# Performance work log

Measured on AMD Instinct MI355X. Metric: run time of the kernel, lower is better.

## Reference

```python
import jax, jax.numpy as jnp
import numpy as np

B, L = 4, 1024
D_MODEL, D_STATE, D_CONV, EXPAND, NUM_HEADS = 512, 64, 4, 2, 8
HEADDIM = 64
D_INNER = EXPAND * D_MODEL          # 1024
NH = D_INNER // HEADDIM             # 16 SSM heads
D_IN_PROJ = 2 * D_INNER + 2 * D_STATE + NH
CONV_DIM = D_INNER + 2 * D_STATE
D_FF = D_MODEL * EXPAND
ADH = D_MODEL // NUM_HEADS          # attn head dim


def setup_inputs() -> dict:
    ks = iter(jax.random.split(jax.random.key(0), 40))
    def rn(shape, s=0.02):
        return jax.random.normal(next(ks), shape, jnp.float32) * s
    return dict(
        x=jax.random.normal(next(ks), (B, L, D_MODEL), jnp.float32),
        g1=jnp.ones(D_MODEL), b1=jnp.zeros(D_MODEL),
        W_in=rn((D_MODEL, D_IN_PROJ)), b_in=jnp.zeros(D_IN_PROJ),
        conv_w=rn((CONV_DIM, D_CONV), 0.1), conv_b=jnp.zeros(CONV_DIM),
        dt_bias=rn((NH,), 0.1), A_log=jnp.zeros(NH), D_skip=jnp.ones(NH),
        gnorm=jnp.ones(D_INNER),
        W_out=rn((D_INNER, D_MODEL)), b_out=jnp.zeros(D_MODEL),
        ga=jnp.ones(D_MODEL), ba=jnp.zeros(D_MODEL),
        Wqkv=rn((D_MODEL, 3 * D_MODEL)), bqkv=jnp.zeros(3 * D_MODEL),
        Wo=rn((D_MODEL, D_MODEL)), bo=jnp.zeros(D_MODEL),
        g2=jnp.ones(D_MODEL), b2=jnp.zeros(D_MODEL),
        W1=rn((D_MODEL, 2 * D_FF)), b1f=jnp.zeros(2 * D_FF),
        W2=rn((D_FF, D_MODEL)), b2f=jnp.zeros(D_MODEL),
    )


def _ln(x, g, b, eps=1e-5):
    mu = x.mean(-1, keepdims=True)
    v = ((x - mu) ** 2).mean(-1, keepdims=True)
    return (x - mu) * jax.lax.rsqrt(v + eps) * g + b


def _ssm(h, W_in, b_in, conv_w, conv_b, dt_bias, A_log, D_skip, gnorm, W_out, b_out):
    # Mamba2: in_proj -> [z | xBC | dt]
    zxbcdt = h @ W_in + b_in
    z = zxbcdt[..., :D_INNER]
    xBC = zxbcdt[..., D_INNER:D_INNER + CONV_DIM]
    dt = jax.nn.softplus(zxbcdt[..., -NH:] + dt_bias)          # [B,L,H]
    # causal depthwise conv (width D_CONV) + SiLU
    xp = jnp.pad(xBC, ((0, 0), (D_CONV - 1, 0), (0, 0)))
    conv = conv_b + sum(xp[:, k:k + L, :] * conv_w[:, k] for k in range(D_CONV))
    xBC = jax.nn.silu(conv)
    bsz = h.shape[0]
    xs = xBC[..., :D_INNER].reshape(bsz, L, NH, HEADDIM)       # [B,L,H,P]
    Bm = xBC[..., D_INNER:D_INNER + D_STATE]                   # [B,L,N]
    Cm = xBC[..., D_INNER + D_STATE:]                          # [B,L,N]
    dA = jnp.exp(dt * (-jnp.exp(A_log)))                       # [B,L,H]
    dtx = dt[..., None] * xs                                   # [B,L,H,P]

    def step(hs, t):
        dA_t, dtx_t, B_t, C_t = t
        hs = hs * dA_t[..., None, None] + dtx_t[..., None] * B_t[:, None, None, :]
        return hs, jnp.einsum('bhpn,bn->bhp', hs, C_t)

    h0 = jnp.zeros((bsz, NH, HEADDIM, D_STATE), h.dtype)
    _, ys = jax.lax.scan(step, h0, (dA.swapaxes(0, 1), dtx.swapaxes(0, 1),
                                     Bm.swapaxes(0, 1), Cm.swapaxes(0, 1)))
    y = ys.swapaxes(0, 1) + D_skip[None, None, :, None] * xs   # [B,L,H,P]
    y = y.reshape(bsz, L, D_INNER) * jax.nn.silu(z)            # gated
    y = y * jax.lax.rsqrt(jnp.mean(y * y, -1, keepdims=True) + 1e-5) * gnorm  # RMSNormGated
    return y @ W_out + b_out


def _attn(h, Wqkv, bqkv, Wo, bo):
    qkv = h @ Wqkv + bqkv
    q, k, v = jnp.split(qkv, 3, axis=-1)
    bsz = h.shape[0]
    rs = lambda t: t.reshape(bsz, L, NUM_HEADS, ADH)
    q, k, v = rs(q), rs(k), rs(v)
    scale = jnp.float32(1.0 / np.sqrt(ADH))
    att = jax.nn.softmax(jnp.einsum('blhd,bmhd->bhlm', q, k) * scale, axis=-1)
    o = jnp.einsum('bhlm,bmhd->blhd', att, v).reshape(bsz, L, D_MODEL)
    return o @ Wo + bo


def _fwd(x, g1, b1, W_in, b_in, conv_w, conv_b, dt_bias, A_log, D_skip, gnorm,
         W_out, b_out, ga, ba, Wqkv, bqkv, Wo, bo, g2, b2, W1, b1f, W2, b2f):
    x = x + _ssm(_ln(x, g1, b1), W_in, b_in, conv_w, conv_b, dt_bias, A_log,
                 D_skip, gnorm, W_out, b_out)
    x = x + _attn(_ln(x, ga, ba), Wqkv, bqkv, Wo, bo)
    h3 = _ln(x, g2, b2)
    x1, x2 = jnp.split(h3 @ W1 + b1f, 2, axis=-1)
    return x + (jax.nn.gelu(x1, approximate=False) * x2) @ W2 + b2f


def reference(x, g1, b1, W_in, b_in, conv_w, conv_b, dt_bias, A_log, D_skip, gnorm,
              W_out, b_out, ga, ba, Wqkv, bqkv, Wo, bo, g2, b2, W1, b1f, W2, b2f):
    return _fwd(x, g1, b1, W_in, b_in, conv_w, conv_b, dt_bias, A_log, D_skip, gnorm,
                W_out, b_out, ga, ba, Wqkv, bqkv, Wo, bo, g2, b2, W1, b1f, W2, b2f)
```

## Files before the change

kernel.cpp:

```cpp
#include <hip/hip_runtime.h>
#include <hip/hip_bf16.h>
#include <math.h>


#define L_      1024
#define DM      512
#define DSTATE  64
#define DCONV   4
#define DINNER  1024
#define NH_     16
#define DINPROJ 2192
#define CONVDIM 1152
#define ROWS    4096
#define LC      64
#define NC      16

typedef float  f32x4  __attribute__((ext_vector_type(4)));
typedef __bf16 bf16x8 __attribute__((ext_vector_type(8)));
typedef short  short8 __attribute__((ext_vector_type(8)));
using bf16 = __hip_bfloat16;

static __device__ __forceinline__ float b2f(ushort u) { return __uint_as_float((unsigned)u << 16); }
static __device__ __forceinline__ ushort f2b(float f) {
  return __builtin_bit_cast(unsigned short, __float2bfloat16(f));
}
static __device__ __forceinline__ void gload16(const void* g, void* l) {
  __builtin_amdgcn_global_load_lds((const __attribute__((address_space(1))) void*)g,
                                   (__attribute__((address_space(3))) void*)l, 16, 0, 0);
}
static __device__ __forceinline__ int swz(int row, int col) {
  return row * 64 + ((((col >> 3) ^ (row & 7)) << 3) | (col & 7));
}

struct TcAll {
  const float* W[6];
  ushort* WT[6];
  int K[6], N[6], Nalloc[6], nbx[6], perm[6];
  int start[7];
};
__global__ __launch_bounds__(256) void tcall_k(TcAll d) {
  int bid = blockIdx.x;
  int i = 0;
  #pragma unroll
  for (int t = 1; t < 6; ++t) if (bid >= d.start[t]) i = t;
  int local = bid - d.start[i];
  int bx = (local % d.nbx[i]) * 32, by = (local / d.nbx[i]) * 32;
  const float* W = d.W[i];
  ushort* WT = d.WT[i];
  int K = d.K[i], N = d.N[i], Nalloc = d.Nalloc[i], pm = d.perm[i];
  __shared__ ushort tile[32][33];
  int tx = threadIdx.x & 31, ty = threadIdx.x >> 5;
  #pragma unroll
  for (int r = ty; r < 32; r += 8) {
    int gk = by + r, gn = bx + tx;
    tile[r][tx] = (gk < K && gn < N) ? f2b(W[(size_t)gk * N + gn]) : (ushort)0;
  }
  __syncthreads();
  #pragma unroll
  for (int r = ty; r < 32; r += 8) {
    int gn = bx + r, gk = by + tx;
    if (gn < Nalloc && gk < K) {
      int gn2 = gn;
      if (pm) gn2 = (gn < 1024) ? ((gn >> 4) * 32 + (gn & 15))
                                : (((gn - 1024) >> 4) * 32 + 16 + ((gn - 1024) & 15));
      WT[(size_t)gn2 * K + gk] = tile[tx][r];
    }
  }
}

__global__ __launch_bounds__(256) void ln512(const float* __restrict__ in, const float* __restrict__ g,
                                             const float* __restrict__ be, bf16* __restrict__ out) {
  int row = blockIdx.x, tid = threadIdx.x;
  const float* x = in + (size_t)row * DM;
  float v0 = x[tid], v1 = x[tid + 256];
  float s = v0 + v1, sq = v0 * v0 + v1 * v1;
  __shared__ float red[4][2];
  __shared__ float bc[2];
  int lane = tid & 63, w = tid >> 6;
  #pragma unroll
  for (int o = 32; o; o >>= 1) { s += __shfl_down(s, o); sq += __shfl_down(sq, o); }
  if (lane == 0) { red[w][0] = s; red[w][1] = sq; }
  __syncthreads();
  if (tid == 0) {
    bc[0] = red[0][0] + red[1][0] + red[2][0] + red[3][0];
    bc[1] = red[0][1] + red[1][1] + red[2][1] + red[3][1];
  }
  __syncthreads();
  float mu = bc[0] * (1.f / DM);
  float var = bc[1] * (1.f / DM) - mu * mu;
  float rs = rsqrtf(var + 1e-5f);
  out[(size_t)row * DM + tid] = __float2bfloat16((v0 - mu) * rs * g[tid] + be[tid]);
  out[(size_t)row * DM + tid + 256] =
      __float2bfloat16((v1 - mu) * rs * g[tid + 256] + be[tid + 256]);
}

template <int OMODE, int BM>
__global__ __launch_bounds__(256) void gemmT(const ushort* __restrict__ A, long lda, long sA1,
                                             const ushort* __restrict__ Bw, long ldb, long sB1,
                                             const float* __restrict__ bias,
                                             void* __restrict__ Cp, long ldc, long sC1,
                                             const float* __restrict__ Rp,
                                             int M, int N, int K, float scale) {
  constexpr int MFR = BM / 32;
  __shared__ ushort As[BM * 64];
  __shared__ ushort Bs[128 * 64];
  const int tid = threadIdx.x;
  const int z = blockIdx.z;
  A  += (size_t)z * sA1;
  Bw += (size_t)z * sB1;
  const int m0 = blockIdx.y * BM, n0 = blockIdx.x * 128;
  const int wave = tid >> 6, lane = tid & 63;
  const int wr = wave >> 1, wc = wave & 1;
  const int frow = lane & 15, fgrp = lane >> 4;

  f32x4 acc[MFR][4];
  #pragma unroll
  for (int m = 0; m < MFR; ++m)
    #pragma unroll
    for (int n = 0; n < 4; ++n) acc[m][n] = {0.f, 0.f, 0.f, 0.f};

  for (int kt = 0; kt < K; kt += 64) {
    #pragma unroll
    for (int it = 0; it < MFR; ++it) {
      int idx = it * 256 + tid;
      int row = idx >> 3, seg = idx & 7;
      gload16(A + (size_t)(m0 + row) * lda + kt + seg * 8, &As[idx * 8]);
    }
    #pragma unroll
    for (int it = 0; it < 4; ++it) {
      int idx = it * 256 + tid;
      int row = idx >> 3, seg = idx & 7;
      gload16(Bw + (size_t)(n0 + row) * ldb + kt + seg * 8, &Bs[idx * 8]);
    }
    __syncthreads();
    #pragma unroll
    for (int kk = 0; kk < 64; kk += 32) {
      bf16x8 af[MFR], bfr[4];
      #pragma unroll
      for (int m = 0; m < MFR; ++m)
        af[m] = *(const bf16x8*)&As[(wr * (BM / 2) + m * 16 + frow) * 64 + kk + 8 * fgrp];
      #pragma unroll
      for (int n = 0; n < 4; ++n)
        bfr[n] = *(const bf16x8*)&Bs[(wc * 64 + n * 16 + frow) * 64 + kk + 8 * fgrp];
      #pragma unroll
      for (int m = 0; m < MFR; ++m)
        #pragma unroll
        for (int n = 0; n < 4; ++n)
          acc[m][n] = __builtin_amdgcn_mfma_f32_16x16x32_bf16(af[m], bfr[n], acc[m][n], 0, 0, 0);
    }
    __syncthreads();
  }

  if (OMODE == 1) {
    #pragma unroll
    for (int jp = 0; jp < 2; ++jp) {
      int oc = n0 / 2 + wc * 32 + jp * 16 + frow;
      float b1v = bias[oc], b2v = bias[1024 + oc];
      #pragma unroll
      for (int m = 0; m < MFR; ++m) {
        #pragma unroll
        for (int r = 0; r < 4; ++r) {
          int gm = m0 + wr * (BM / 2) + m * 16 + fgrp * 4 + r;
          float x1 = acc[m][jp * 2][r] + b1v;
          float x2 = acc[m][jp * 2 + 1][r] + b2v;
          float g = 0.5f * x1 * (1.f + erff(x1 * 0.70710678f));
          ((bf16*)Cp)[(size_t)gm * ldc + oc] = __float2bfloat16(g * x2);
        }
      }
    }
    return;
  }
  #pragma unroll
  for (int n = 0; n < 4; ++n) {
    int gn = n0 + wc * 64 + n * 16 + frow;
    if (gn >= N) continue;
    float bv = bias ? bias[gn] : 0.f;
    #pragma unroll
    for (int m = 0; m < MFR; ++m) {
      #pragma unroll
      for (int r = 0; r < 4; ++r) {
        int gm = m0 + wr * (BM / 2) + m * 16 + fgrp * 4 + r;
        float v = acc[m][n][r] * scale + bv;
        size_t off = (size_t)z * sC1 + (size_t)gm * ldc + gn;
        if (OMODE == 0)      ((bf16*)Cp)[off] = __float2bfloat16(v);
        else if (OMODE == 2) ((float*)Cp)[off] += v;
        else                 ((float*)Cp)[off] = Rp[off] + v;
      }
    }
  }
}

__global__ __launch_bounds__(256) void fattn_k(const ushort* __restrict__ qkv,
                                               const ushort* __restrict__ VT,
                                               ushort* __restrict__ Opart,
                                               float* __restrict__ lpart) {
  const int qt = blockIdx.x, bh = blockIdx.y, z = blockIdx.z, b = bh >> 3, hh = bh & 7;
  const int tid = threadIdx.x, wave = tid >> 6, lane = tid & 63;
  const int frow = lane & 15, fgrp = lane >> 4;
  __shared__ __align__(16) ushort QP_lds[64 * 64];
  __shared__ __align__(16) ushort K_lds[2][64 * 64];
  __shared__ __align__(16) ushort V_lds[2][64 * 64];
  const int q0 = qt * 64;
  const int kv0 = z * 4;
  const int r0 = tid >> 3, r1 = r0 + 32, sg = (tid & 7) * 8;

  *(short8*)&QP_lds[swz(r0, sg)] =
      *(const short8*)(qkv + (size_t)(b * L_ + q0 + r0) * 1536 + hh * 64 + sg);
  *(short8*)&QP_lds[swz(r1, sg)] =
      *(const short8*)(qkv + (size_t)(b * L_ + q0 + r1) * 1536 + hh * 64 + sg);
  __syncthreads();
  bf16x8 qf[2];
  qf[0] = *(const bf16x8*)&QP_lds[swz(wave * 16 + frow, 8 * fgrp)];
  qf[1] = *(const bf16x8*)&QP_lds[swz(wave * 16 + frow, 32 + 8 * fgrp)];

  float l_r[4] = {0.f, 0.f, 0.f, 0.f};
  f32x4 o_acc[4];
  #pragma unroll
  for (int j = 0; j < 4; ++j) o_acc[j] = {0.f, 0.f, 0.f, 0.f};

  short8 kr0, kr1, vr0, vr1;
  {
    const ushort* kp = qkv + (size_t)(b * L_ + kv0 * 64) * 1536 + 512 + hh * 64;
    kr0 = *(const short8*)(kp + (size_t)r0 * 1536 + sg);
    kr1 = *(const short8*)(kp + (size_t)r1 * 1536 + sg);
    const ushort* vp = VT + (size_t)bh * 65536 + kv0 * 64;
    vr0 = *(const short8*)(vp + (size_t)r0 * 1024 + sg);
    vr1 = *(const short8*)(vp + (size_t)r1 * 1024 + sg);
  }

  for (int kv = kv0; kv < kv0 + 4; ++kv) {
    const int cur = kv & 1;
    *(short8*)&K_lds[cur][swz(r0, sg)] = kr0;
    *(short8*)&K_lds[cur][swz(r1, sg)] = kr1;
    *(short8*)&V_lds[cur][swz(r0, sg)] = vr0;
    *(short8*)&V_lds[cur][swz(r1, sg)] = vr1;
    __syncthreads();
    if (kv < kv0 + 3) {
      const ushort* kp = qkv + (size_t)(b * L_ + (kv + 1) * 64) * 1536 + 512 + hh * 64;
      kr0 = *(const short8*)(kp + (size_t)r0 * 1536 + sg);
      kr1 = *(const short8*)(kp + (size_t)r1 * 1536 + sg);
      const ushort* vp = VT + (size_t)bh * 65536 + (kv + 1) * 64;
      vr0 = *(const short8*)(vp + (size_t)r0 * 1024 + sg);
      vr1 = *(const short8*)(vp + (size_t)r1 * 1024 + sg);
    }

    f32x4 s[4];
    #pragma unroll
    for (int j = 0; j < 4; ++j) s[j] = {0.f, 0.f, 0.f, 0.f};
    #pragma unroll
    for (int kk = 0; kk < 2; ++kk) {
      bf16x8 a = qf[kk];
      #pragma unroll
      for (int j = 0; j < 4; ++j) {
        bf16x8 bb = *(const bf16x8*)&K_lds[cur][swz(j * 16 + frow, kk * 32 + 8 * fgrp)];
        s[j] = __builtin_amdgcn_mfma_f32_16x16x32_bf16(a, bb, s[j], 0, 0, 0);
      }
    }
    #pragma unroll
    for (int r = 0; r < 4; ++r) {
      #pragma unroll
      for (int j = 0; j < 4; ++j) {
        float p = __expf(s[j][r] * 0.125f);
        s[j][r] = p;
        l_r[r] += p;
      }
    }
    #pragma unroll
    for (int r = 0; r < 4; ++r)
      #pragma unroll
      for (int j = 0; j < 4; ++j)
        QP_lds[swz(wave * 16 + fgrp * 4 + r, j * 16 + frow)] = f2b(s[j][r]);
    #pragma unroll
    for (int kk = 0; kk < 2; ++kk) {
      bf16x8 pa = *(const bf16x8*)&QP_lds[swz(wave * 16 + frow, kk * 32 + 8 * fgrp)];
      #pragma unroll
      for (int j = 0; j < 4; ++j) {
        bf16x8 bb = *(const bf16x8*)&V_lds[cur][swz(j * 16 + frow, kk * 32 + 8 * fgrp)];
        o_acc[j] = __builtin_amdgcn_mfma_f32_16x16x32_bf16(pa, bb, o_acc[j], 0, 0, 0);
      }
    }
  }
  #pragma unroll
  for (int r = 0; r < 4; ++r) {
    #pragma unroll
    for (int o = 1; o < 16; o <<= 1) l_r[r] += __shfl_xor(l_r[r], o);
  }
  ushort* Op = Opart + (size_t)z * ROWS * DM;
  #pragma unroll
  for (int r = 0; r < 4; ++r) {
    int orow = q0 + wave * 16 + fgrp * 4 + r;
    #pragma unroll
    for (int j = 0; j < 4; ++j)
      Op[(size_t)(b * L_ + orow) * DM + hh * 64 + j * 16 + frow] = f2b(o_acc[j][r]);
    if (frow == 0) lpart[(size_t)z * ROWS * 8 + (size_t)(b * L_ + orow) * 8 + hh] = l_r[r];
  }
}

__global__ __launch_bounds__(256) void fcomb_k(const ushort* __restrict__ Opart,
                                               const float* __restrict__ lpart,
                                               bf16* __restrict__ Out) {
  int i = blockIdx.x * 256 + threadIdx.x;
  int row = i >> 7, c4 = (i & 127) * 4;
  int hh = c4 >> 6;
  float acc[4] = {0.f, 0.f, 0.f, 0.f};
  float l = 0.f;
  #pragma unroll
  for (int z = 0; z < 4; ++z) {
    ushort4 u = *(const ushort4*)&Opart[(size_t)z * ROWS * DM + (size_t)row * DM + c4];
    acc[0] += b2f(u.x); acc[1] += b2f(u.y); acc[2] += b2f(u.z); acc[3] += b2f(u.w);
    l += lpart[(size_t)z * ROWS * 8 + (size_t)row * 8 + hh];
  }
  float inv = 1.f / l;
  ushort4 o;
  o.x = f2b(acc[0] * inv); o.y = f2b(acc[1] * inv);
  o.z = f2b(acc[2] * inv); o.w = f2b(acc[3] * inv);
  *(ushort4*)&Out[(size_t)row * DM + c4] = o;
}

__global__ __launch_bounds__(256) void convk(const ushort* __restrict__ zx, const float* __restrict__ cw,
                                             const float* __restrict__ cb, ushort* __restrict__ xbc) {
  const int rt = blockIdx.x;
  const int t = rt & (L_ - 1);
  const int tid = threadIdx.x;
  const ushort* zrow = zx + (size_t)rt * DINPROJ + DINNER;
  ushort* xrow = xbc + (size_t)rt * CONVDIM;
  for (int cc = tid * 4; cc < CONVDIM; cc += 1024) {
    float4 w0 = *(const float4*)&cw[cc * 4];
    float4 w1 = *(const float4*)&cw[cc * 4 + 4];
    float4 w2 = *(const float4*)&cw[cc * 4 + 8];
    float4 w3 = *(const float4*)&cw[cc * 4 + 12];
    float4 bias = *(const float4*)&cb[cc];
    float a0 = bias.x, a1 = bias.y, a2 = bias.z, a3 = bias.w;
    #pragma unroll
    for (int k = 0; k < DCONV; ++k) {
      int dt_ = k - 3;
      if (t + dt_ >= 0) {
        ushort4 v = *(const ushort4*)(zrow + (long)dt_ * DINPROJ + cc);
        a0 += b2f(v.x) * ((const float*)&w0)[k];
        a1 += b2f(v.y) * ((const float*)&w1)[k];
        a2 += b2f(v.z) * ((const float*)&w2)[k];
        a3 += b2f(v.w) * ((const float*)&w3)[k];
      }
    }
    ushort4 o;
    o.x = f2b(a0 / (1.f + __expf(-a0)));
    o.y = f2b(a1 / (1.f + __expf(-a1)));
    o.z = f2b(a2 / (1.f + __expf(-a2)));
    o.w = f2b(a3 / (1.f + __expf(-a3)));
    *(ushort4*)(xrow + cc) = o;
  }
}

__global__ __launch_bounds__(256) void scanA_k(const ushort* __restrict__ xbc,
                                               const ushort* __restrict__ zx,
                                               const float* __restrict__ dtb,
                                               const float* __restrict__ alog,
                                               ushort* __restrict__ Sbuf,
                                               float* __restrict__ Pbuf,
                                               float* __restrict__ laBuf,
                                               float* __restrict__ dtBuf) {
  const int c = blockIdx.x, bh = blockIdx.y, b = bh >> 4, hh = bh & 15;
  const int tid = threadIdx.x, wave = tid >> 6, lane = tid & 63;
  const int frow = lane & 15, fgrp = lane >> 4;
  const int t0 = c * LC;
  __shared__ __align__(16) ushort XT[64][72];
  __shared__ __align__(16) ushort BT[64][72];
  __shared__ float sw[64];

  if (tid < 64) {
    int row = b * L_ + t0 + tid;
    float v = b2f(zx[(size_t)row * DINPROJ + (DINPROJ - NH_) + hh]) + dtb[hh];
    float d = (v > 20.f) ? v : log1pf(__expf(v));
    float la = -__expf(alog[hh]) * d;
    #pragma unroll
    for (int off = 1; off < 64; off <<= 1) {
      float u = __shfl_up(la, off);
      if (tid >= off) la += u;
    }
    float la63 = __shfl(la, 63);
    sw[tid] = d * __expf(la63 - la);
    laBuf[((size_t)bh * NC + c) * 64 + tid] = la;
    dtBuf[((size_t)bh * NC + c) * 64 + tid] = d;
    if (tid == 63) Pbuf[bh * NC + c] = __expf(la);
  }
  __syncthreads();

  {
    int t = tid >> 2, ch0 = (tid & 3) * 16;
    size_t base = (size_t)(b * L_ + t0 + t) * CONVDIM;
    short8 x0 = *(const short8*)&xbc[base + hh * 64 + ch0];
    short8 x1 = *(const short8*)&xbc[base + hh * 64 + ch0 + 8];
    short8 b0 = *(const short8*)&xbc[base + DINNER + ch0];
    short8 b1 = *(const short8*)&xbc[base + DINNER + ch0 + 8];
    float wt = sw[t];
    #pragma unroll
    for (int j = 0; j < 8; ++j) {
      XT[ch0 + j][t]     = f2b(b2f((ushort)x0[j]) * wt);
      XT[ch0 + 8 + j][t] = f2b(b2f((ushort)x1[j]) * wt);
      BT[ch0 + j][t]     = (ushort)b0[j];
      BT[ch0 + 8 + j][t] = (ushort)b1[j];
    }
  }
  __syncthreads();

  f32x4 acc[4];
  #pragma unroll
  for (int j = 0; j < 4; ++j) acc[j] = {0.f, 0.f, 0.f, 0.f};
  #pragma unroll
  for (int kk = 0; kk < 2; ++kk) {
    bf16x8 a = *(const bf16x8*)&XT[wave * 16 + frow][kk * 32 + 8 * fgrp];
    #pragma unroll
    for (int j = 0; j < 4; ++j) {
      bf16x8 bb = *(const bf16x8*)&BT[j * 16 + frow][kk * 32 + 8 * fgrp];
      acc[j] = __builtin_amdgcn_mfma_f32_16x16x32_bf16(a, bb, acc[j], 0, 0, 0);
    }
  }
  ushort* Sp = Sbuf + ((size_t)bh * NC + c) * 4096;
  #pragma unroll
  for (int j = 0; j < 4; ++j)
    #pragma unroll
    for (int r = 0; r < 4; ++r)
      Sp[(wave * 16 + fgrp * 4 + r) * 64 + j * 16 + frow] = f2b(acc[j][r]);
}

__global__ __launch_bounds__(256) void scanB_k(const ushort* __restrict__ xbc,
                                               const float* __restrict__ Dskip,
                                               const ushort* __restrict__ Sbuf,
                                               const float* __restrict__ Pbuf,
                                               const float* __restrict__ laBuf,
                                               const float* __restrict__ dtBuf,
                                               ushort* __restrict__ yb) {
  const int c = blockIdx.x, bh = blockIdx.y, b = bh >> 4, hh = bh & 15;
  const int tid = threadIdx.x, wave = tid >> 6, lane = tid & 63;
  const int frow = lane & 15, fgrp = lane >> 4;
  const int t0 = c * LC;
  __shared__ __align__(16) ushort C_l[64][72];
  __shared__ __align__(16) ushort BH[64][72];
  __shared__ __align__(16) ushort XT[64][72];
  __shared__ __align__(16) ushort M_l[64][72];
  __shared__ float sla[64], sdt[64];

  if (tid < 64) {
    sla[tid] = laBuf[((size_t)bh * NC + c) * 64 + tid];
    sdt[tid] = dtBuf[((size_t)bh * NC + c) * 64 + tid];
  }
  {
    int t = tid >> 2, ch0 = (tid & 3) * 16;
    size_t base = (size_t)(b * L_ + t0 + t) * CONVDIM;
    short8 c0 = *(const short8*)&xbc[base + DINNER + DSTATE + ch0];
    short8 c1 = *(const short8*)&xbc[base + DINNER + DSTATE + ch0 + 8];
    *(short8*)&C_l[t][ch0] = c0;
    *(short8*)&C_l[t][ch0 + 8] = c1;
    short8 b0 = *(const short8*)&xbc[base + DINNER + ch0];
    short8 b1 = *(const short8*)&xbc[base + DINNER + ch0 + 8];
    *(short8*)&BH[t][ch0] = b0;
    *(short8*)&BH[t][ch0 + 8] = b1;
    short8 x0 = *(const short8*)&xbc[base + hh * 64 + ch0];
    short8 x1 = *(const short8*)&xbc[base + hh * 64 + ch0 + 8];
    #pragma unroll
    for (int j = 0; j < 8; ++j) {
      XT[ch0 + j][t]     = (ushort)x0[j];
      XT[ch0 + 8 + j][t] = (ushort)x1[j];
    }
  }
  float Hreg[16];
  #pragma unroll
  for (int j = 0; j < 16; ++j) Hreg[j] = 0.f;
  {
    int p = tid >> 2, n0 = (tid & 3) * 16;
    for (int cc = 0; cc < c; ++cc) {
      const ushort* Sp = Sbuf + ((size_t)bh * NC + cc) * 4096 + p * 64 + n0;
      float P = Pbuf[bh * NC + cc];
      short8 a = *(const short8*)Sp;
      short8 bq = *(const short8*)(Sp + 8);
      #pragma unroll
      for (int j = 0; j < 8; ++j) {
        Hreg[j]     = Hreg[j]     * P + b2f((ushort)a[j]);
        Hreg[8 + j] = Hreg[8 + j] * P + b2f((ushort)bq[j]);
      }
    }
  }
  __syncthreads();

  f32x4 g[4];
  #pragma unroll
  for (int j = 0; j < 4; ++j) g[j] = {0.f, 0.f, 0.f, 0.f};
  #pragma unroll
  for (int kk = 0; kk < 2; ++kk) {
    bf16x8 a = *(const bf16x8*)&C_l[wave * 16 + frow][kk * 32 + 8 * fgrp];
    #pragma unroll
    for (int j = 0; j < 4; ++j) {
      bf16x8 bb = *(const bf16x8*)&BH[j * 16 + frow][kk * 32 + 8 * fgrp];
      g[j] = __builtin_amdgcn_mfma_f32_16x16x32_bf16(a, bb, g[j], 0, 0, 0);
    }
  }
  #pragma unroll
  for (int r = 0; r < 4; ++r) {
    int trow = wave * 16 + fgrp * 4 + r;
    float lat = sla[trow];
    #pragma unroll
    for (int j = 0; j < 4; ++j) {
      int scol = j * 16 + frow;
      float m = (scol <= trow) ? __expf(lat - sla[scol]) * sdt[scol] * g[j][r] : 0.f;
      M_l[trow][scol] = f2b(m);
    }
  }
  __syncthreads();
  {
    int p = tid >> 2, n0 = (tid & 3) * 16;
    short8 w0, w1;
    #pragma unroll
    for (int j = 0; j < 8; ++j) { w0[j] = (short)f2b(Hreg[j]); w1[j] = (short)f2b(Hreg[8 + j]); }
    *(short8*)&BH[p][n0] = w0;
    *(short8*)&BH[p][n0 + 8] = w1;
  }
  __syncthreads();

  f32x4 y1[4], y2[4];
  #pragma unroll
  for (int j = 0; j < 4; ++j) { y1[j] = {0.f, 0.f, 0.f, 0.f}; y2[j] = {0.f, 0.f, 0.f, 0.f}; }
  #pragma unroll
  for (int kk = 0; kk < 2; ++kk) {
    bf16x8 am = *(const bf16x8*)&M_l[wave * 16 + frow][kk * 32 + 8 * fgrp];
    bf16x8 ac = *(const bf16x8*)&C_l[wave * 16 + frow][kk * 32 + 8 * fgrp];
    #pragma unroll
    for (int j = 0; j < 4; ++j) {
      bf16x8 bx = *(const bf16x8*)&XT[j * 16 + frow][kk * 32 + 8 * fgrp];
      bf16x8 bhf = *(const bf16x8*)&BH[j * 16 + frow][kk * 32 + 8 * fgrp];
      y1[j] = __builtin_amdgcn_mfma_f32_16x16x32_bf16(am, bx, y1[j], 0, 0, 0);
      y2[j] = __builtin_amdgcn_mfma_f32_16x16x32_bf16(ac, bhf, y2[j], 0, 0, 0);
    }
  }
  float dsk = Dskip[hh];
  #pragma unroll
  for (int r = 0; r < 4; ++r) {
    int trow = wave * 16 + fgrp * 4 + r;
    float ea = __expf(sla[trow]);
    size_t orow = (size_t)(b * L_ + t0 + trow) * DINNER + hh * 64;
    #pragma unroll
    for (int j = 0; j < 4; ++j) {
      int pcol = j * 16 + frow;
      float y = y1[j][r] + ea * y2[j][r] + dsk * b2f(XT[pcol][trow]);
      yb[orow + pcol] = f2b(y);
    }
  }
}

__global__ __launch_bounds__(256) void grms_k(const ushort* __restrict__ yb, const ushort* __restrict__ zx,
                                              const float* __restrict__ gn, bf16* __restrict__ out) {
  int row = blockIdx.x, tid = threadIdx.x;
  const ushort* y = yb + (size_t)row * DINNER;
  const ushort* z = zx + (size_t)row * DINPROJ;
  float v[4], sq = 0.f;
  #pragma unroll
  for (int k = 0; k < 4; ++k) {
    int c = tid + k * 256;
    float zz = b2f(z[c]);
    float val = b2f(y[c]) * (zz / (1.f + __expf(-zz)));
    v[k] = val;
    sq += val * val;
  }
  __shared__ float red[4];
  __shared__ float bc;
  int lane = tid & 63, w = tid >> 6;
  #pragma unroll
  for (int o = 32; o; o >>= 1) sq += __shfl_down(sq, o);
  if (lane == 0) red[w] = sq;
  __syncthreads();
  if (tid == 0) bc = red[0] + red[1] + red[2] + red[3];
  __syncthreads();
  float rs = rsqrtf(bc * (1.f / DINNER) + 1e-5f);
  #pragma unroll
  for (int k = 0; k < 4; ++k) {
    int c = tid + k * 256;
    out[(size_t)row * DINNER + c] = __float2bfloat16(v[k] * rs * gn[c]);
  }
}

__global__ __launch_bounds__(256) void vt_k(const ushort* __restrict__ qkv, ushort* __restrict__ VT) {
  int bh = blockIdx.z, b = bh >> 3, hh = bh & 7;
  int m0 = blockIdx.x * 32, d0 = blockIdx.y * 32;
  __shared__ ushort tile[32][33];
  int tx = threadIdx.x & 31, ty = threadIdx.x >> 5;
  #pragma unroll
  for (int r = ty; r < 32; r += 8)
    tile[r][tx] = qkv[(size_t)(b * L_ + m0 + r) * 1536 + 1024 + hh * 64 + d0 + tx];
  __syncthreads();
  #pragma unroll
  for (int r = ty; r < 32; r += 8)
    VT[(size_t)bh * 65536 + (size_t)(d0 + r) * 1024 + m0 + tx] = tile[tx][r];
}

extern "C" void kernel_launch(void* const* d_in, const int* in_sizes, int n_in,
                              void* d_out, int out_size, void* d_ws, size_t ws_size,
                              hipStream_t stream) {
  const float* x_in = (const float*)d_in[0];
  const float* g1   = (const float*)d_in[1];
  const float* b1   = (const float*)d_in[2];
  const float* b_in = (const float*)d_in[4];
  const float* cw   = (const float*)d_in[5];
  const float* cb   = (const float*)d_in[6];
  const float* dtb  = (const float*)d_in[7];
  const float* alog = (const float*)d_in[8];
  const float* dsk  = (const float*)d_in[9];
  const float* gno  = (const float*)d_in[10];
  const float* bout = (const float*)d_in[12];
  const float* ga   = (const float*)d_in[13];
  const float* ba   = (const float*)d_in[14];
  const float* bqkv = (const float*)d_in[16];
  const float* bo   = (const float*)d_in[18];
  const float* g2   = (const float*)d_in[19];
  const float* b2   = (const float*)d_in[20];
  const float* b1f  = (const float*)d_in[22];
  const float* b2f_ = (const float*)d_in[24];

  char* ws = (char*)d_ws;
  ushort* WT_in  = (ushort*)(ws + 0);
  ushort* WT_out = (ushort*)(ws + 2359296);
  ushort* WT_qkv = (ushort*)(ws + 3407872);
  ushort* WT_o   = (ushort*)(ws + 4980736);
  ushort* WT_1   = (ushort*)(ws + 5505024);
  ushort* WT_2   = (ushort*)(ws + 7602176);
  float*  r   = (float*)(ws + 8650752);
  bf16*   h   = (bf16*)(ws + 17039360);
  ushort* zx  = (ushort*)(ws + 21233664);
  ushort* xbc = (ushort*)(ws + 39190528);
  ushort* yb  = (ushort*)(ws + 49152000);
  bf16*   hy  = (bf16*)(ws + 57540608);
  ushort* qkv = zx;
  ushort* Sbuf = (ushort*)hy;
  ushort* VT   = (ushort*)hy;
  float*  Pbuf  = (float*)h;
  float*  laBuf = (float*)((char*)h + 65536);
  float*  dtBuf = (float*)((char*)h + 327680);
  ushort* Opart = (ushort*)(ws + 39190528);
  float*  lpart = (float*)(ws + 55967744);

  TcAll tc;
  tc.W[0] = (const float*)d_in[3];  tc.WT[0] = WT_in;  tc.K[0] = 512;  tc.N[0] = 2192; tc.Nalloc[0] = 2304; tc.nbx[0] = 72; tc.perm[0] = 0;
  tc.W[1] = (const float*)d_in[11]; tc.WT[1] = WT_out; tc.K[1] = 1024; tc.N[1] = 512;  tc.Nalloc[1] = 512;  tc.nbx[1] = 16; tc.perm[1] = 0;
  tc.W[2] = (const float*)d_in[15]; tc.WT[2] = WT_qkv; tc.K[2] = 512;  tc.N[2] = 1536; tc.Nalloc[2] = 1536; tc.nbx[2] = 48; tc.perm[2] = 0;
  tc.W[3] = (const float*)d_in[17]; tc.WT[3] = WT_o;   tc.K[3] = 512;  tc.N[3] = 512;  tc.Nalloc[3] = 512;  tc.nbx[3] = 16; tc.perm[3] = 0;
  tc.W[4] = (const float*)d_in[21]; tc.WT[4] = WT_1;   tc.K[4] = 512;  tc.N[4] = 2048; tc.Nalloc[4] = 2048; tc.nbx[4] = 64; tc.perm[4] = 1;
  tc.W[5] = (const float*)d_in[23]; tc.WT[5] = WT_2;   tc.K[5] = 1024; tc.N[5] = 512;  tc.Nalloc[5] = 512;  tc.nbx[5] = 16; tc.perm[5] = 0;
  tc.start[0] = 0;    tc.start[1] = 1152; tc.start[2] = 1664; tc.start[3] = 2432;
  tc.start[4] = 2688; tc.start[5] = 3712; tc.start[6] = 4224;
  tcall_k<<<4224, 256, 0, stream>>>(tc);

  ln512<<<ROWS, 256, 0, stream>>>(x_in, g1, b1, h);
  gemmT<0, 64><<<dim3(18, 64, 1), 256, 0, stream>>>((const ushort*)h, 512, 0, WT_in, 512, 0,
                                                    b_in, zx, 2192, 0, nullptr, 4096, 2192, 512, 1.f);
  convk<<<ROWS, 256, 0, stream>>>(zx, cw, cb, xbc);
  scanA_k<<<dim3(NC, 64), 256, 0, stream>>>(xbc, zx, dtb, alog, Sbuf, Pbuf, laBuf, dtBuf);
  scanB_k<<<dim3(NC, 64), 256, 0, stream>>>(xbc, dsk, Sbuf, Pbuf, laBuf, dtBuf, yb);
  grms_k<<<ROWS, 256, 0, stream>>>(yb, zx, gno, hy);
  gemmT<3, 64><<<dim3(4, 64, 1), 256, 0, stream>>>((const ushort*)hy, 1024, 0, WT_out, 1024, 0,
                                                   bout, r, 512, 0, x_in, 4096, 512, 1024, 1.f);
  ln512<<<ROWS, 256, 0, stream>>>(r, ga, ba, h);
  gemmT<0, 64><<<dim3(12, 64, 1), 256, 0, stream>>>((const ushort*)h, 512, 0, WT_qkv, 512, 0,
                                                    bqkv, qkv, 1536, 0, nullptr, 4096, 1536, 512, 1.f);
  vt_k<<<dim3(32, 2, 32), 256, 0, stream>>>(qkv, (ushort*)VT);
  fattn_k<<<dim3(16, 32, 4), 256, 0, stream>>>(qkv, (const ushort*)VT, Opart, lpart);
  fcomb_k<<<2048, 256, 0, stream>>>(Opart, lpart, h);
  gemmT<2, 64><<<dim3(4, 64, 1), 256, 0, stream>>>((const ushort*)h, 512, 0, WT_o, 512, 0,
                                                   bo, r, 512, 0, nullptr, 4096, 512, 512, 1.f);
  ln512<<<ROWS, 256, 0, stream>>>(r, g2, b2, h);
  gemmT<1, 64><<<dim3(16, 64, 1), 256, 0, stream>>>((const ushort*)h, 512, 0, WT_1, 512, 0,
                                                    b1f, hy, 1024, 0, nullptr, 4096, 2048, 512, 1.f);
  gemmT<3, 64><<<dim3(4, 64, 1), 256, 0, stream>>>((const ushort*)hy, 1024, 0, WT_2, 1024, 0,
                                                   b2f_, d_out, 512, 0, r, 4096, 512, 1024, 1.f);
}
```

Baseline: 224.8 us.

## Fuse gated RMSNorm into out-proj GEMM and V transpose into QKV epilogue

Replaces the separate gated-RMSNorm kernel with a new GEMM kernel that computes y*silu(z)*gnorm on the fly while loading A tiles, accumulates per-row sum of squares, and applies the rsqrt scale in the epilogue before adding bias and residual. Also adds a GEMM epilogue mode that writes the V part of QKV directly in transposed layout, removing the vt_k kernel. This removes two launches and the intermediate global round-trips of hy and the V transpose. In exchange, the norm scale is applied after the bf16 rounding of the unnormalized product, which changes rounding. The out-proj blocks also recompute the SiLU gating redundantly across the 4 N-tiles, and the A loads are no longer async.

```diff
diff --git a/kernel.cpp b/kernel.cpp
--- a/kernel.cpp
+++ b/kernel.cpp
@@ -100,6 +100,7 @@
                                              const float* __restrict__ bias,
                                              void* __restrict__ Cp, long ldc, long sC1,
                                              const float* __restrict__ Rp,
+                                             ushort* __restrict__ VTp,
                                              int M, int N, int K, float scale) {
   constexpr int MFR = BM / 32;
   __shared__ ushort As[BM * 64];
@@ -170,6 +171,29 @@
     }
     return;
   }
+  if (OMODE == 4) {
+    #pragma unroll
+    for (int n = 0; n < 4; ++n) {
+      int gnv = n0 + wc * 64 + n * 16 + frow;
+      float bv = bias[gnv];
+      #pragma unroll
+      for (int m = 0; m < MFR; ++m) {
+        int gm0 = m0 + wr * (BM / 2) + m * 16 + fgrp * 4;
+        if (gnv < 1024) {
+          #pragma unroll
+          for (int r = 0; r < 4; ++r)
+            ((bf16*)Cp)[(size_t)(gm0 + r) * ldc + gnv] = __float2bfloat16(acc[m][n][r] + bv);
+        } else {
+          int d = (gnv - 1024) & 63, hh2 = (gnv - 1024) >> 6, bb = gm0 >> 10;
+          ushort4 u;
+          u.x = f2b(acc[m][n][0] + bv); u.y = f2b(acc[m][n][1] + bv);
+          u.z = f2b(acc[m][n][2] + bv); u.w = f2b(acc[m][n][3] + bv);
+          *(ushort4*)&VTp[((size_t)(bb * 8 + hh2) * 64 + d) * 1024 + (gm0 & 1023)] = u;
+        }
+      }
+    }
+    return;
+  }
   #pragma unroll
   for (int n = 0; n < 4; ++n) {
     int gn = n0 + wc * 64 + n * 16 + frow;
@@ -185,6 +209,114 @@
         if (OMODE == 0)      ((bf16*)Cp)[off] = __float2bfloat16(v);
         else if (OMODE == 2) ((float*)Cp)[off] += v;
         else                 ((float*)Cp)[off] = Rp[off] + v;
+      }
+    }
+  }
+}
+
+__global__ __launch_bounds__(256) void gemmW_k(const ushort* __restrict__ yb,
+                                               const ushort* __restrict__ zx,
+                                               const float* __restrict__ gnorm,
+                                               const float* __restrict__ bout,
+                                               const ushort* __restrict__ Bw,
+                                               const float* __restrict__ xin,
+                                               float* __restrict__ rout) {
+  __shared__ __align__(16) ushort As[64][72];
+  __shared__ ushort Bs[128 * 64];
+  __shared__ float rs_l[64];
+  const int tid = threadIdx.x;
+  const int m0 = blockIdx.y * 64, n0 = blockIdx.x * 128;
+  const int wave = tid >> 6, lane = tid & 63;
+  const int wr = wave >> 1, wc = wave & 1;
+  const int frow = lane & 15, fgrp = lane >> 4;
+  const int r0 = tid >> 3, r1 = r0 + 32, sg = (tid & 7) * 8;
+
+  f32x4 acc[2][4];
+  #pragma unroll
+  for (int m = 0; m < 2; ++m)
+    #pragma unroll
+    for (int n = 0; n < 4; ++n) acc[m][n] = {0.f, 0.f, 0.f, 0.f};
+  float sq0 = 0.f, sq1 = 0.f;
+
+  for (int kt = 0; kt < 1024; kt += 64) {
+    #pragma unroll
+    for (int it = 0; it < 4; ++it) {
+      int idx = it * 256 + tid;
+      int row = idx >> 3, seg = idx & 7;
+      gload16(Bw + (size_t)(n0 + row) * 1024 + kt + seg * 8, &Bs[idx * 8]);
+    }
+    {
+      short8 yv = *(const short8*)(yb + (size_t)(m0 + r0) * DINNER + kt + sg);
+      short8 zv = *(const short8*)(zx + (size_t)(m0 + r0) * DINPROJ + kt + sg);
+      float4 ga = *(const float4*)&gnorm[kt + sg];
+      float4 gb = *(const float4*)&gnorm[kt + sg + 4];
+      short8 o;
+      #pragma unroll
+      for (int j = 0; j < 8; ++j) {
+        float zz = b2f((ushort)zv[j]);
+        float val = b2f((ushort)yv[j]) * (zz / (1.f + __expf(-zz)));
+        sq0 += val * val;
+        float gv = (j < 4) ? ((const float*)&ga)[j] : ((const float*)&gb)[j - 4];
+        o[j] = (short)f2b(val * gv);
+      }
+      *(short8*)&As[r0][sg] = o;
+    }
+    {
+      short8 yv = *(const short8*)(yb + (size_t)(m0 + r1) * DINNER + kt + sg);
+      short8 zv = *(const short8*)(zx + (size_t)(m0 + r1) * DINPROJ + kt + sg);
+      float4 ga = *(const float4*)&gnorm[kt + sg];
+      float4 gb = *(const float4*)&gnorm[kt + sg + 4];
+      short8 o;
+      #pragma unroll
+      for (int j = 0; j < 8; ++j) {
+        float zz = b2f((ushort)zv[j]);
+        float val = b2f((ushort)yv[j]) * (zz / (1.f + __expf(-zz)));
+        sq1 += val * val;
+        float gv = (j < 4) ? ((const float*)&ga)[j] : ((const float*)&gb)[j - 4];
+        o[j] = (short)f2b(val * gv);
+      }
+      *(short8*)&As[r1][sg] = o;
+    }
+    __syncthreads();
+    #pragma unroll
+    for (int kk = 0; kk < 64; kk += 32) {
+      bf16x8 af[2], bfr[4];
+      #pragma unroll
+      for (int m = 0; m < 2; ++m)
+        af[m] = *(const bf16x8*)&As[wr * 32 + m * 16 + frow][kk + 8 * fgrp];
+      #pragma unroll
+      for (int n = 0; n < 4; ++n)
+        bfr[n] = *(const bf16x8*)&Bs[(wc * 64 + n * 16 + frow) * 64 + kk + 8 * fgrp];
+      #pragma unroll
+      for (int m = 0; m < 2; ++m)
+        #pragma unroll
+        for (int n = 0; n < 4; ++n)
+          acc[m][n] = __builtin_amdgcn_mfma_f32_16x16x32_bf16(af[m], bfr[n], acc[m][n], 0, 0, 0);
+    }
+    __syncthreads();
+  }
+  #pragma unroll
+  for (int o = 1; o < 8; o <<= 1) {
+    sq0 += __shfl_xor(sq0, o);
+    sq1 += __shfl_xor(sq1, o);
+  }
+  if ((tid & 7) == 0) {
+    rs_l[r0] = rsqrtf(sq0 * (1.f / DINNER) + 1e-5f);
+    rs_l[r1] = rsqrtf(sq1 * (1.f / DINNER) + 1e-5f);
+  }
+  __syncthreads();
+  #pragma unroll
+  for (int n = 0; n < 4; ++n) {
+    int gn = n0 + wc * 64 + n * 16 + frow;
+    float bv = bout[gn];
+    #pragma unroll
+    for (int m = 0; m < 2; ++m) {
+      #pragma unroll
+      for (int r = 0; r < 4; ++r) {
+        int lm = wr * 32 + m * 16 + fgrp * 4 + r;
+        int gm = m0 + lm;
+        size_t off = (size_t)gm * DM + gn;
+        rout[off] = xin[off] + acc[m][n][r] * rs_l[lm] + bv;
       }
     }
   }
@@ -544,51 +676,6 @@
       yb[orow + pcol] = f2b(y);
     }
   }
-}
-
-__global__ __launch_bounds__(256) void grms_k(const ushort* __restrict__ yb, const ushort* __restrict__ zx,
-                                              const float* __restrict__ gn, bf16* __restrict__ out) {
-  int row = blockIdx.x, tid = threadIdx.x;
-  const ushort* y = yb + (size_t)row * DINNER;
-  const ushort* z = zx + (size_t)row * DINPROJ;
-  float v[4], sq = 0.f;
-  #pragma unroll
-  for (int k = 0; k < 4; ++k) {
-    int c = tid + k * 256;
-    float zz = b2f(z[c]);
-    float val = b2f(y[c]) * (zz / (1.f + __expf(-zz)));
-    v[k] = val;
-    sq += val * val;
-  }
-  __shared__ float red[4];
-  __shared__ float bc;
-  int lane = tid & 63, w = tid >> 6;
-  #pragma unroll
-  for (int o = 32; o; o >>= 1) sq += __shfl_down(sq, o);
-  if (lane == 0) red[w] = sq;
-  __syncthreads();
-  if (tid == 0) bc = red[0] + red[1] + red[2] + red[3];
-  __syncthreads();
-  float rs = rsqrtf(bc * (1.f / DINNER) + 1e-5f);
-  #pragma unroll
-  for (int k = 0; k < 4; ++k) {
-    int c = tid + k * 256;
-    out[(size_t)row * DINNER + c] = __float2bfloat16(v[k] * rs * gn[c]);
-  }
-}
-
-__global__ __launch_bounds__(256) void vt_k(const ushort* __restrict__ qkv, ushort* __restrict__ VT) {
-  int bh = blockIdx.z, b = bh >> 3, hh = bh & 7;
-  int m0 = blockIdx.x * 32, d0 = blockIdx.y * 32;
-  __shared__ ushort tile[32][33];
-  int tx = threadIdx.x & 31, ty = threadIdx.x >> 5;
-  #pragma unroll
-  for (int r = ty; r < 32; r += 8)
-    tile[r][tx] = qkv[(size_t)(b * L_ + m0 + r) * 1536 + 1024 + hh * 64 + d0 + tx];
-  __syncthreads();
-  #pragma unroll
-  for (int r = ty; r < 32; r += 8)
-    VT[(size_t)bh * 65536 + (size_t)(d0 + r) * 1024 + m0 + tx] = tile[tx][r];
 }
 
 extern "C" void kernel_launch(void* const* d_in, const int* in_sizes, int n_in,
@@ -649,24 +736,26 @@
 
   ln512<<<ROWS, 256, 0, stream>>>(x_in, g1, b1, h);
   gemmT<0, 64><<<dim3(18, 64, 1), 256, 0, stream>>>((const ushort*)h, 512, 0, WT_in, 512, 0,
-                                                    b_in, zx, 2192, 0, nullptr, 4096, 2192, 512, 1.f);
+                                                    b_in, zx, 2192, 0, nullptr, nullptr,
+                                                    4096, 2192, 512, 1.f);
   convk<<<ROWS, 256, 0, stream>>>(zx, cw, cb, xbc);
   scanA_k<<<dim3(NC, 64), 256, 0, stream>>>(xbc, zx, dtb, alog, Sbuf, Pbuf, laBuf, dtBuf);
   scanB_k<<<dim3(NC, 64), 256, 0, stream>>>(xbc, dsk, Sbuf, Pbuf, laBuf, dtBuf, yb);
-  grms_k<<<ROWS, 256, 0, stream>>>(yb, zx, gno, hy);
-  gemmT<3, 64><<<dim3(4, 64, 1), 256, 0, stream>>>((const ushort*)hy, 1024, 0, WT_out, 1024, 0,
-                                                   bout, r, 512, 0, x_in, 4096, 512, 1024, 1.f);
+  gemmW_k<<<dim3(4, 64), 256, 0, stream>>>(yb, zx, gno, bout, WT_out, x_in, r);
   ln512<<<ROWS, 256, 0, stream>>>(r, ga, ba, h);
-  gemmT<0, 64><<<dim3(12, 64, 1), 256, 0, stream>>>((const ushort*)h, 512, 0, WT_qkv, 512, 0,
-                                                    bqkv, qkv, 1536, 0, nullptr, 4096, 1536, 512, 1.f);
-  vt_k<<<dim3(32, 2, 32), 256, 0, stream>>>(qkv, (ushort*)VT);
+  gemmT<4, 64><<<dim3(12, 64, 1), 256, 0, stream>>>((const ushort*)h, 512, 0, WT_qkv, 512, 0,
+                                                    bqkv, qkv, 1536, 0, nullptr, (ushort*)VT,
+                                                    4096, 1536, 512, 1.f);
   fattn_k<<<dim3(16, 32, 4), 256, 0, stream>>>(qkv, (const ushort*)VT, Opart, lpart);
   fcomb_k<<<2048, 256, 0, stream>>>(Opart, lpart, h);
   gemmT<2, 64><<<dim3(4, 64, 1), 256, 0, stream>>>((const ushort*)h, 512, 0, WT_o, 512, 0,
-                                                   bo, r, 512, 0, nullptr, 4096, 512, 512, 1.f);
+                                                   bo, r, 512, 0, nullptr, nullptr,
+                                                   4096, 512, 512, 1.f);
   ln512<<<ROWS, 256, 0, stream>>>(r, g2, b2, h);
   gemmT<1, 64><<<dim3(16, 64, 1), 256, 0, stream>>>((const ushort*)h, 512, 0, WT_1, 512, 0,
-                                                    b1f, hy, 1024, 0, nullptr, 4096, 2048, 512, 1.f);
+                                                    b1f, hy, 1024, 0, nullptr, nullptr,
+                                                    4096, 2048, 512, 1.f);
   gemmT<3, 64><<<dim3(4, 64, 1), 256, 0, stream>>>((const ushort*)hy, 1024, 0, WT_2, 1024, 0,
-                                                   b2f_, d_out, 512, 0, r, 4096, 512, 1024, 1.f);
-}
+                                                   b2f_, d_out, 512, 0, r, nullptr,
+                                                   4096, 512, 1024, 1.f);
+}
```

After: 228.0 us. Within noise of the previous version (+1.4%).
